# Kernel tuning notes

Hardware: AMD Instinct MI355X
Metric: run time of the kernel (lower is better)

The kernel has to match this reference:

```python
import jax, jax.numpy as jnp
import numpy as np

D_MODEL, D_K, C_DIM = 1024, 64, 64
B, S = 4, 4096


def setup_inputs() -> dict:
    key = jax.random.key(0)
    ks = jax.random.split(key, 10)
    sc = 1.0 / np.sqrt(D_MODEL)
    return {
        "X": jax.random.normal(ks[0], (B, S, D_MODEL), jnp.float32),
        "cultural_embedding": jax.random.normal(ks[1], (B, C_DIM), jnp.float32),
        "WQ": jax.random.normal(ks[2], (D_MODEL, D_K), jnp.float32) * sc,
        "bQ": jnp.zeros((D_K,), jnp.float32),
        "WK": jax.random.normal(ks[3], (D_MODEL, D_K), jnp.float32) * sc,
        "bK": jnp.zeros((D_K,), jnp.float32),
        "WV": jax.random.normal(ks[4], (D_MODEL, D_K), jnp.float32) * sc,
        "bV": jnp.zeros((D_K,), jnp.float32),
        "WC": jax.random.normal(ks[5], (C_DIM, D_K), jnp.float32) * (1.0 / np.sqrt(C_DIM)),
        "bC": jnp.zeros((D_K,), jnp.float32),
        "lam": jnp.float32(1.0),
    }


def reference(X, cultural_embedding, WQ, bQ, WK, bK, WV, bV, WC, bC, lam):
    # Projections: [B,S,d_k]
    Q = jnp.einsum('bsm,mk->bsk', X, WQ) + bQ
    K = jnp.einsum('bsm,mk->bsk', X, WK) + bK
    V = jnp.einsum('bsm,mk->bsk', X, WV) + bV
    # Cultural projection: [B,d_k]
    c_proj = cultural_embedding @ WC + bC
    # Base attention logits [B,S,S]
    base_logits = jnp.einsum('bqk,bsk->bqs', Q, K) / jnp.sqrt(jnp.float32(D_K))
    # Rank-1 cultural bias per query row, scalar lambda gate
    cultural_bias = lam * jnp.einsum('bsd,bd->bs', Q, c_proj)  # [B,S]
    combined = base_logits + cultural_bias[..., None]
    attn = jax.nn.softmax(combined, axis=-1)
    return jnp.einsum('bqs,bsk->bqk', attn, V)
```

## Files before the change

kernel.cpp:

```cpp
#include <hip/hip_runtime.h>

#define B_  4
#define S_  4096
#define DM  1024
#define DK  64
#define NSPLIT 8
#define KSPAN (S_ / NSPLIT)
#define QT  256

typedef _Float16 half8  __attribute__((ext_vector_type(8)));
typedef _Float16 half4v __attribute__((ext_vector_type(4)));
typedef float    floatx4 __attribute__((ext_vector_type(4)));

#define QSCALE 0.18033688011112042f
#define EXP2F(x) __builtin_amdgcn_exp2f(x)

__global__ __launch_bounds__(256) void wt_kernel(
    const float* __restrict__ WQ, const float* __restrict__ WK,
    const float* __restrict__ WV, _Float16* __restrict__ Wt)
{
    const int proj = blockIdx.y;
    const float* W = (proj == 0) ? WQ : (proj == 1) ? WK : WV;
    const int k0 = blockIdx.x * 64;
    const int t = threadIdx.x;
    __shared__ float T[64][68];

    #pragma unroll
    for (int p = 0; p < 4; p++) {
        int c = p * 256 + t;
        int k = c >> 4, n4 = (c & 15) * 4;
        float4 v = *(const float4*)(W + (size_t)(k0 + k) * DK + n4);
        T[k][n4 + 0] = v.x; T[k][n4 + 1] = v.y;
        T[k][n4 + 2] = v.z; T[k][n4 + 3] = v.w;
    }
    __syncthreads();

    const int n = t >> 2, kc = (t & 3) * 16;
    half8 h0, h1;
    #pragma unroll
    for (int j = 0; j < 8; j++) h0[j] = (_Float16)T[kc + j][n];
    #pragma unroll
    for (int j = 0; j < 8; j++) h1[j] = (_Float16)T[kc + 8 + j][n];
    _Float16* dst = Wt + ((size_t)proj * 64 + n) * DM + k0 + kc;
    *(half8*)(dst)     = h0;
    *(half8*)(dst + 8) = h1;
}

__global__ __launch_bounds__(256) void proj_mfma_kernel(
    const float* __restrict__ X, const _Float16* __restrict__ Wt,
    const float* __restrict__ bQ, const float* __restrict__ bK,
    const float* __restrict__ bV,
    _Float16* __restrict__ Qh, _Float16* __restrict__ Kh,
    _Float16* __restrict__ Vt)
{
    const int r0   = blockIdx.x * 64;
    const int t    = threadIdx.x;
    const int wave = t >> 6, lane = t & 63;
    const int quad = lane >> 4, l15 = lane & 15;

    __shared__ __align__(16) _Float16 Xs[64 * 72];
    __shared__ __align__(16) _Float16 Ws[3][64 * 72];

    floatx4 acc[3][4];
    #pragma unroll
    for (int p = 0; p < 3; p++)
        #pragma unroll
        for (int nt = 0; nt < 4; nt++)
            acc[p][nt] = (floatx4){0.f, 0.f, 0.f, 0.f};

    int xrow[4], xcol[4];
    #pragma unroll
    for (int p = 0; p < 4; p++) {
        int c = p * 256 + t;
        xrow[p] = c >> 4; xcol[p] = (c & 15) * 4;
    }
    int wrow[2], wcol[2];
    #pragma unroll
    for (int p = 0; p < 2; p++) {
        int c = p * 256 + t;
        wrow[p] = c >> 3; wcol[p] = (c & 7) * 8;
    }

    float4 xr[4]; half8 wr[3][2];
    #pragma unroll
    for (int p = 0; p < 4; p++)
        xr[p] = *(const float4*)(X + (size_t)(r0 + xrow[p]) * DM + xcol[p]);
    #pragma unroll
    for (int pr = 0; pr < 3; pr++)
        #pragma unroll
        for (int p = 0; p < 2; p++)
            wr[pr][p] = *(const half8*)(Wt + ((size_t)pr * 64 + wrow[p]) * DM + wcol[p]);

    for (int kt = 0; kt < DM / 64; kt++) {
        __syncthreads();
        #pragma unroll
        for (int p = 0; p < 4; p++) {
            half4v h;
            h[0] = (_Float16)xr[p].x; h[1] = (_Float16)xr[p].y;
            h[2] = (_Float16)xr[p].z; h[3] = (_Float16)xr[p].w;
            *(half4v*)&Xs[xrow[p] * 72 + xcol[p]] = h;
        }
        #pragma unroll
        for (int pr = 0; pr < 3; pr++)
            #pragma unroll
            for (int p = 0; p < 2; p++)
                *(half8*)&Ws[pr][wrow[p] * 72 + wcol[p]] = wr[pr][p];
        __syncthreads();

        if (kt + 1 < DM / 64) {
            const int kn = (kt + 1) * 64;
            #pragma unroll
            for (int p = 0; p < 4; p++)
                xr[p] = *(const float4*)(X + (size_t)(r0 + xrow[p]) * DM + kn + xcol[p]);
            #pragma unroll
            for (int pr = 0; pr < 3; pr++)
                #pragma unroll
                for (int p = 0; p < 2; p++)
                    wr[pr][p] = *(const half8*)(Wt + ((size_t)pr * 64 + wrow[p]) * DM + kn + wcol[p]);
        }

        half8 xa0 = *(half8*)&Xs[(wave * 16 + l15) * 72 + quad * 8];
        half8 xa1 = *(half8*)&Xs[(wave * 16 + l15) * 72 + 32 + quad * 8];
        #pragma unroll
        for (int pr = 0; pr < 3; pr++) {
            #pragma unroll
            for (int nt = 0; nt < 4; nt++) {
                half8 bf0 = *(half8*)&Ws[pr][(nt * 16 + l15) * 72 + quad * 8];
                half8 bf1 = *(half8*)&Ws[pr][(nt * 16 + l15) * 72 + 32 + quad * 8];
                floatx4 a = acc[pr][nt];
                a = __builtin_amdgcn_mfma_f32_16x16x32_f16(xa0, bf0, a, 0, 0, 0);
                a = __builtin_amdgcn_mfma_f32_16x16x32_f16(xa1, bf1, a, 0, 0, 0);
                acc[pr][nt] = a;
            }
        }
    }

    float bqv[4], bkv[4], bvv[4];
    #pragma unroll
    for (int nt = 0; nt < 4; nt++) {
        bqv[nt] = bQ[nt * 16 + l15];
        bkv[nt] = bK[nt * 16 + l15];
        bvv[nt] = bV[nt * 16 + l15];
    }

    const int orow = r0 + wave * 16 + quad * 4;
    const int bidx = r0 >> 12;
    const int s0   = (r0 & (S_ - 1)) + wave * 16 + quad * 4;
    #pragma unroll
    for (int nt = 0; nt < 4; nt++) {
        const int d = nt * 16 + l15;
        #pragma unroll
        for (int i = 0; i < 4; i++) {
            Qh[(size_t)(orow + i) * DK + d] =
                (_Float16)((acc[0][nt][i] + bqv[nt]) * QSCALE);
            Kh[(size_t)(orow + i) * DK + d] =
                (_Float16)(acc[1][nt][i] + bkv[nt]);
        }
        half4v hv;
        #pragma unroll
        for (int i = 0; i < 4; i++)
            hv[i] = (_Float16)(acc[2][nt][i] + bvv[nt]);
        *(half4v*)(Vt + (size_t)bidx * DK * S_ + (size_t)d * S_ + s0) = hv;
    }
}

__global__ __launch_bounds__(512, 4) void flash_mfma_kernel(
    const _Float16* __restrict__ Qh, const _Float16* __restrict__ Kh,
    const _Float16* __restrict__ Vt, _Float16* __restrict__ Oph,
    float* __restrict__ Lp)
{
    const int b     = blockIdx.y;
    const int q0    = blockIdx.x * QT;
    const int split = blockIdx.z;
    const int kbase = split * KSPAN;
    const int t     = threadIdx.x;
    const int wave  = t >> 6, lane = t & 63;
    const int quad  = lane >> 4, l15 = lane & 15;

    __shared__ __align__(16) _Float16 Ks[64 * 72];
    __shared__ __align__(16) _Float16 Vs[64 * 72];
    __shared__ __align__(16) _Float16 QsPs[QT * 72];

    const _Float16* Qb = Qh + ((size_t)b * S_ + q0) * DK;
    const _Float16* Kb = Kh + ((size_t)b * S_ + kbase) * DK;
    const _Float16* Vb = Vt + (size_t)b * DK * S_ + kbase;

    #pragma unroll
    for (int p = 0; p < 4; p++) {
        int c = p * 512 + t;
        int r = c >> 3, col = (c & 7) * 8;
        *(half8*)&QsPs[r * 72 + col] = *(const half8*)(Qb + r * 64 + col);
    }
    __syncthreads();
    half8 qf0[2], qf1[2];
    #pragma unroll
    for (int mt = 0; mt < 2; mt++) {
        const int r = wave * 32 + mt * 16 + l15;
        qf0[mt] = *(half8*)&QsPs[r * 72 + quad * 8];
        qf1[mt] = *(half8*)&QsPs[r * 72 + 32 + quad * 8];
    }
    __syncthreads();

    _Float16* Pw = &QsPs[wave * 32 * 72];

    floatx4 acc[2][4];
    float rs[2][4];
    #pragma unroll
    for (int mt = 0; mt < 2; mt++) {
        #pragma unroll
        for (int nt = 0; nt < 4; nt++) acc[mt][nt] = (floatx4){0.f,0.f,0.f,0.f};
        #pragma unroll
        for (int i = 0; i < 4; i++) rs[mt][i] = 0.f;
    }

    const int kr = t >> 3, kcol = (t & 7) * 8;
    half8 kreg = *(const half8*)(Kb + (size_t)kr * DK + kcol);
    half8 vreg = *(const half8*)(Vb + (size_t)kr * S_ + kcol);

    for (int k0 = 0; k0 < KSPAN; k0 += 64) {
        __syncthreads();
        *(half8*)&Ks[kr * 72 + kcol] = kreg;
        *(half8*)&Vs[kr * 72 + kcol] = vreg;
        __syncthreads();

        const int kn = k0 + 64;
        if (kn < KSPAN) {
            kreg = *(const half8*)(Kb + (size_t)(kn + kr) * DK + kcol);
            vreg = *(const half8*)(Vb + (size_t)kr * S_ + kn + kcol);
        }

        floatx4 sc[2][4];
        #pragma unroll
        for (int nt = 0; nt < 4; nt++) {
            half8 kf0 = *(half8*)&Ks[(nt * 16 + l15) * 72 + quad * 8];
            half8 kf1 = *(half8*)&Ks[(nt * 16 + l15) * 72 + 32 + quad * 8];
            #pragma unroll
            for (int mt = 0; mt < 2; mt++) {
                floatx4 z = (floatx4){0.f, 0.f, 0.f, 0.f};
                z = __builtin_amdgcn_mfma_f32_16x16x32_f16(qf0[mt], kf0, z, 0, 0, 0);
                z = __builtin_amdgcn_mfma_f32_16x16x32_f16(qf1[mt], kf1, z, 0, 0, 0);
                sc[mt][nt] = z;
            }
        }

        #pragma unroll
        for (int mt = 0; mt < 2; mt++)
            #pragma unroll
            for (int nt = 0; nt < 4; nt++)
                #pragma unroll
                for (int i = 0; i < 4; i++) {
                    float pe = EXP2F(sc[mt][nt][i]);
                    rs[mt][i] += pe;
                    Pw[(mt * 16 + quad * 4 + i) * 72 + nt * 16 + l15] = (_Float16)pe;
                }

        half8 pf0[2], pf1[2];
        #pragma unroll
        for (int mt = 0; mt < 2; mt++) {
            pf0[mt] = *(half8*)&Pw[(mt * 16 + l15) * 72 + quad * 8];
            pf1[mt] = *(half8*)&Pw[(mt * 16 + l15) * 72 + 32 + quad * 8];
        }

        #pragma unroll
        for (int nt = 0; nt < 4; nt++) {
            half8 vf0 = *(half8*)&Vs[(nt * 16 + l15) * 72 + quad * 8];
            half8 vf1 = *(half8*)&Vs[(nt * 16 + l15) * 72 + 32 + quad * 8];
            #pragma unroll
            for (int mt = 0; mt < 2; mt++) {
                floatx4 a = acc[mt][nt];
                a = __builtin_amdgcn_mfma_f32_16x16x32_f16(pf0[mt], vf0, a, 0, 0, 0);
                a = __builtin_amdgcn_mfma_f32_16x16x32_f16(pf1[mt], vf1, a, 0, 0, 0);
                acc[mt][nt] = a;
            }
        }
    }

    const size_t prow = (size_t)split * B_ * S_ + (size_t)b * S_ + q0;
    #pragma unroll
    for (int mt = 0; mt < 2; mt++) {
        float inv[4];
        #pragma unroll
        for (int i = 0; i < 4; i++) {
            float r = rs[mt][i];
            #pragma unroll
            for (int off = 1; off < 16; off <<= 1)
                r += __shfl_xor(r, off, 64);
            rs[mt][i] = r;
            inv[i] = 1.0f / r;
        }
        const int rbase = wave * 32 + mt * 16 + quad * 4;
        #pragma unroll
        for (int nt = 0; nt < 4; nt++)
            #pragma unroll
            for (int i = 0; i < 4; i++)
                Oph[(prow + rbase + i) * DK + nt * 16 + l15] =
                    (_Float16)(acc[mt][nt][i] * inv[i]);
        if (l15 == 0) {
            #pragma unroll
            for (int i = 0; i < 4; i++)
                Lp[prow + rbase + i] = rs[mt][i];
        }
    }
}

__global__ __launch_bounds__(256) void combine_kernel(
    const _Float16* __restrict__ Oph, const float* __restrict__ Lp,
    float* __restrict__ O)
{
    const int r  = blockIdx.x * 16 + (threadIdx.x >> 4);
    const int d4 = (threadIdx.x & 15) * 4;
    const int NR = B_ * S_;

    float lw[NSPLIT], lsum = 0.f;
    #pragma unroll
    for (int s = 0; s < NSPLIT; s++) {
        lw[s] = Lp[(size_t)s * NR + r];
        lsum += lw[s];
    }
    const float inv = 1.0f / lsum;

    float o[4] = {0.f, 0.f, 0.f, 0.f};
    #pragma unroll
    for (int s = 0; s < NSPLIT; s++) {
        half4v h = *(const half4v*)(Oph + ((size_t)s * NR + r) * DK + d4);
        const float w = lw[s];
        #pragma unroll
        for (int j = 0; j < 4; j++) o[j] += w * (float)h[j];
    }
    float4 out;
    out.x = o[0] * inv; out.y = o[1] * inv;
    out.z = o[2] * inv; out.w = o[3] * inv;
    *(float4*)(O + (size_t)r * DK + d4) = out;
}

extern "C" void kernel_launch(void* const* d_in, const int* in_sizes, int n_in,
                              void* d_out, int out_size, void* d_ws, size_t ws_size,
                              hipStream_t stream)
{
    const float* X  = (const float*)d_in[0];
    const float* WQ = (const float*)d_in[2];
    const float* bQ = (const float*)d_in[3];
    const float* WK = (const float*)d_in[4];
    const float* bK = (const float*)d_in[5];
    const float* WV = (const float*)d_in[6];
    const float* bV = (const float*)d_in[7];

    char* ws = (char*)d_ws;
    _Float16* Qh  = (_Float16*)ws;  ws += (size_t)B_ * S_ * DK * 2;
    _Float16* Kh  = (_Float16*)ws;  ws += (size_t)B_ * S_ * DK * 2;
    _Float16* Vt  = (_Float16*)ws;  ws += (size_t)B_ * S_ * DK * 2;
    _Float16* Wt  = (_Float16*)ws;  ws += (size_t)3 * 64 * DM * 2;
    _Float16* Oph = (_Float16*)ws;  ws += (size_t)NSPLIT * B_ * S_ * DK * 2;
    float* Lp     = (float*)ws;

    wt_kernel<<<dim3(DM / 64, 3), 256, 0, stream>>>(WQ, WK, WV, Wt);

    proj_mfma_kernel<<<dim3((B_ * S_) / 64), 256, 0, stream>>>(
        X, Wt, bQ, bK, bV, Qh, Kh, Vt);

    flash_mfma_kernel<<<dim3(S_ / QT, B_, NSPLIT), 512, 0, stream>>>(
        Qh, Kh, Vt, Oph, Lp);

    combine_kernel<<<dim3((B_ * S_) / 16), 256, 0, stream>>>(
        Oph, Lp, (float*)d_out);
}
```

Baseline: 154.9 us.

## Double-buffer K/V tiles in LDS and shrink per-wave P scratch

```diff
diff --git a/kernel.cpp b/kernel.cpp
--- a/kernel.cpp
+++ b/kernel.cpp
@@ -177,31 +177,23 @@
     const int wave  = t >> 6, lane = t & 63;
     const int quad  = lane >> 4, l15 = lane & 15;
 
-    __shared__ __align__(16) _Float16 Ks[64 * 72];
-    __shared__ __align__(16) _Float16 Vs[64 * 72];
-    __shared__ __align__(16) _Float16 QsPs[QT * 72];
+    __shared__ __align__(16) _Float16 Ks[2][64 * 72];
+    __shared__ __align__(16) _Float16 Vs[2][64 * 72];
+    __shared__ __align__(16) _Float16 Ps[8][16 * 72];
 
     const _Float16* Qb = Qh + ((size_t)b * S_ + q0) * DK;
     const _Float16* Kb = Kh + ((size_t)b * S_ + kbase) * DK;
     const _Float16* Vb = Vt + (size_t)b * DK * S_ + kbase;
 
-    #pragma unroll
-    for (int p = 0; p < 4; p++) {
-        int c = p * 512 + t;
-        int r = c >> 3, col = (c & 7) * 8;
-        *(half8*)&QsPs[r * 72 + col] = *(const half8*)(Qb + r * 64 + col);
-    }
-    __syncthreads();
     half8 qf0[2], qf1[2];
     #pragma unroll
     for (int mt = 0; mt < 2; mt++) {
-        const int r = wave * 32 + mt * 16 + l15;
-        qf0[mt] = *(half8*)&QsPs[r * 72 + quad * 8];
-        qf1[mt] = *(half8*)&QsPs[r * 72 + 32 + quad * 8];
-    }
-    __syncthreads();
-
-    _Float16* Pw = &QsPs[wave * 32 * 72];
+        const _Float16* qr = Qb + (size_t)(wave * 32 + mt * 16 + l15) * DK;
+        qf0[mt] = *(const half8*)(qr + quad * 8);
+        qf1[mt] = *(const half8*)(qr + 32 + quad * 8);
+    }
+
+    _Float16* Pw = &Ps[wave][0];
 
     floatx4 acc[2][4];
     float rs[2][4];
@@ -216,24 +208,26 @@
     const int kr = t >> 3, kcol = (t & 7) * 8;
     half8 kreg = *(const half8*)(Kb + (size_t)kr * DK + kcol);
     half8 vreg = *(const half8*)(Vb + (size_t)kr * S_ + kcol);
-
-    for (int k0 = 0; k0 < KSPAN; k0 += 64) {
+    *(half8*)&Ks[0][kr * 72 + kcol] = kreg;
+    *(half8*)&Vs[0][kr * 72 + kcol] = vreg;
+
+    const int NT = KSPAN / 64;
+    int cur = 0;
+    for (int it = 0; it < NT; it++) {
         __syncthreads();
-        *(half8*)&Ks[kr * 72 + kcol] = kreg;
-        *(half8*)&Vs[kr * 72 + kcol] = vreg;
-        __syncthreads();
-
-        const int kn = k0 + 64;
-        if (kn < KSPAN) {
+
+        if (it + 1 < NT) {
+            const int kn = (it + 1) * 64;
             kreg = *(const half8*)(Kb + (size_t)(kn + kr) * DK + kcol);
             vreg = *(const half8*)(Vb + (size_t)kr * S_ + kn + kcol);
         }
 
         floatx4 sc[2][4];
+        __builtin_amdgcn_s_setprio(1);
         #pragma unroll
         for (int nt = 0; nt < 4; nt++) {
-            half8 kf0 = *(half8*)&Ks[(nt * 16 + l15) * 72 + quad * 8];
-            half8 kf1 = *(half8*)&Ks[(nt * 16 + l15) * 72 + 32 + quad * 8];
+            half8 kf0 = *(half8*)&Ks[cur][(nt * 16 + l15) * 72 + quad * 8];
+            half8 kf1 = *(half8*)&Ks[cur][(nt * 16 + l15) * 72 + 32 + quad * 8];
             #pragma unroll
             for (int mt = 0; mt < 2; mt++) {
                 floatx4 z = (floatx4){0.f, 0.f, 0.f, 0.f};
@@ -242,29 +236,28 @@
                 sc[mt][nt] = z;
             }
         }
-
-        #pragma unroll
-        for (int mt = 0; mt < 2; mt++)
+        __builtin_amdgcn_s_setprio(0);
+
+        half8 pf0[2], pf1[2];
+        #pragma unroll
+        for (int mt = 0; mt < 2; mt++) {
             #pragma unroll
             for (int nt = 0; nt < 4; nt++)
                 #pragma unroll
                 for (int i = 0; i < 4; i++) {
                     float pe = EXP2F(sc[mt][nt][i]);
                     rs[mt][i] += pe;
-                    Pw[(mt * 16 + quad * 4 + i) * 72 + nt * 16 + l15] = (_Float16)pe;
+                    Pw[(quad * 4 + i) * 72 + nt * 16 + l15] = (_Float16)pe;
                 }
-
-        half8 pf0[2], pf1[2];
-        #pragma unroll
-        for (int mt = 0; mt < 2; mt++) {
-            pf0[mt] = *(half8*)&Pw[(mt * 16 + l15) * 72 + quad * 8];
-            pf1[mt] = *(half8*)&Pw[(mt * 16 + l15) * 72 + 32 + quad * 8];
-        }
-
+            pf0[mt] = *(half8*)&Pw[l15 * 72 + quad * 8];
+            pf1[mt] = *(half8*)&Pw[l15 * 72 + 32 + quad * 8];
+        }
+
+        __builtin_amdgcn_s_setprio(1);
         #pragma unroll
         for (int nt = 0; nt < 4; nt++) {
-            half8 vf0 = *(half8*)&Vs[(nt * 16 + l15) * 72 + quad * 8];
-            half8 vf1 = *(half8*)&Vs[(nt * 16 + l15) * 72 + 32 + quad * 8];
+            half8 vf0 = *(half8*)&Vs[cur][(nt * 16 + l15) * 72 + quad * 8];
+            half8 vf1 = *(half8*)&Vs[cur][(nt * 16 + l15) * 72 + 32 + quad * 8];
             #pragma unroll
             for (int mt = 0; mt < 2; mt++) {
                 floatx4 a = acc[mt][nt];
@@ -273,6 +266,13 @@
                 acc[mt][nt] = a;
             }
         }
+        __builtin_amdgcn_s_setprio(0);
+
+        if (it + 1 < NT) {
+            *(half8*)&Ks[cur ^ 1][kr * 72 + kcol] = kreg;
+            *(half8*)&Vs[cur ^ 1][kr * 72 + kcol] = vreg;
+        }
+        cur ^= 1;
     }
 
     const size_t prow = (size_t)split * B_ * S_ + (size_t)b * S_ + q0;
```

Result: no change. 155.0 us (+0.1%).
